# Optimization experiments

Measured on AMD Instinct MI355X. Metric: run time of the kernel, lower is better.

The kernel has to match this reference:

```python
import jax, jax.numpy as jnp
import numpy as np

B, IN_DIM, H, OUT_DIM = 2048, 1024, 256, 512   # batch, input_dim, hidden_dim, output_dim
T, K, HOPS = 12, 3, 4                            # num_tempers, ops per temper, max_path_hops


def setup_inputs() -> dict:
    key = jax.random.key(0)
    ks = jax.random.split(key, 10)
    s = 0.02
    return dict(
        x=jax.random.normal(ks[0], (B, IN_DIM), jnp.float32),
        init_tempers=jax.random.randint(ks[1], (B,), 0, T),
        op_noise=jax.random.normal(ks[2], (HOPS, T, K), jnp.float32),
        route_u=jax.random.uniform(ks[3], (HOPS, B, T + 1), jnp.float32),
        W_in=jax.random.normal(ks[4], (IN_DIM, H), jnp.float32) * s,
        b_in=jnp.zeros((H,), jnp.float32),
        W1=jax.random.normal(ks[5], (T, K, H, H), jnp.float32) * s,
        b1=jnp.zeros((T, K, H), jnp.float32),
        W2=jax.random.normal(ks[6], (T, K, H, H), jnp.float32) * s,
        b2=jnp.zeros((T, K, H), jnp.float32),
        Wr=jax.random.normal(ks[7], (T, H, T + 1), jnp.float32) * s,
        br=jnp.zeros((T, T + 1), jnp.float32),
        W_out=jax.random.normal(ks[8], (H, OUT_DIM), jnp.float32) * s,
        b_out=jnp.zeros((OUT_DIM,), jnp.float32),
    )


def reference(x, init_tempers, op_noise, route_u, W_in, b_in, W1, b1, W2, b2, Wr, br, W_out, b_out):
    # input projection; num_patches = hidden//hidden = 1, so patches == x_proj [N, H]
    states = x @ W_in + b_in                      # [N, H]
    N = states.shape[0]
    tempers = init_tempers                        # [N] in [0, T)
    done = jnp.zeros((N,), dtype=bool)

    for hop in range(HOPS):
        # per-temper operator mixing weights: softmax over randn(3) per Temper call
        w = jax.nn.softmax(op_noise[hop], axis=-1)                      # [T, K]
        # run all T expert MLPs densely (static-shape MoE dispatch), combine via one-hot
        h1 = jax.nn.relu(jnp.einsum('nh,tkhd->tnkd', states, W1) + b1[:, None])   # [T, N, K, H]
        h2 = jax.nn.relu(jnp.einsum('tnkd,tkdf->tnkf', h1, W2) + b2[:, None])     # [T, N, K, H]
        out_t = jnp.einsum('tnkf,tk->tnf', h2, w)                                  # [T, N, H]
        logits_t = jnp.einsum('tnf,tfg->tng', out_t, Wr) + br[:, None]             # [T, N, T+1]
        sel = jax.nn.one_hot(tempers, T, dtype=states.dtype)                       # [N, T]
        out = jnp.einsum('tnf,nt->nf', out_t, sel)                                 # [N, H]
        logits = jnp.einsum('tng,nt->ng', logits_t, sel)                           # [N, T+1]
        # multinomial(softmax(logits)) == argmax(logits + Gumbel)
        g = -jnp.log(-jnp.log(route_u[hop] + 1e-9) + 1e-9)
        sampled = jnp.argmax(logits + g, axis=-1)                                  # [N]
        active = ~done
        states = jnp.where(active[:, None], out, states)
        tempers = jnp.where(active, jnp.minimum(sampled, T - 1), tempers)
        done = done | (active & (sampled == T))

    # view(B, 1, H).mean(dim=1) is identity since num_patches == 1
    return states @ W_out + b_out
```

## Files before the change

kernel.cpp:

```cpp
#include <hip/hip_runtime.h>
#include <math.h>

#define BN_   2048
#define INDIM 1024
#define HD    256
#define OD    512
#define TN    12
#define KN    3
#define NHOPS 4
#define TP1   13

#define ER    8
#define CR    16

__device__ __forceinline__ void gll16(const float* g, float* l) {
  __builtin_amdgcn_global_load_lds(
      (const __attribute__((address_space(1))) void*)g,
      (__attribute__((address_space(3))) void*)l, 16, 0, 0);
}

__device__ __forceinline__ float4 ld4(const float* p) { return *(const float4*)p; }

__device__ __forceinline__ void fma4(float4& c, float a, const float4 b) {
  c.x = fmaf(a, b.x, c.x); c.y = fmaf(a, b.y, c.y);
  c.z = fmaf(a, b.z, c.z); c.w = fmaf(a, b.w, c.w);
}
__device__ __forceinline__ void add4(float4& c, const float4 b) {
  c.x += b.x; c.y += b.y; c.z += b.z; c.w += b.w;
}

template<int NR>
__device__ __forceinline__ void kloop(float4* acc, const float* SA, int astr,
                                      const float* w0, int ws, int nk4, int ks0) {
  const float* wp = w0;
  float4 wA0 = ld4(wp), wA1 = ld4(wp + ws), wA2 = ld4(wp + 2 * ws),
         wA3 = ld4(wp + 3 * ws);
#pragma unroll 1
  for (int k4 = 0; k4 < nk4 - 1; ++k4) {
    const float* wn = wp + 4 * ws;
    float4 wB0 = ld4(wn), wB1 = ld4(wn + ws), wB2 = ld4(wn + 2 * ws),
           wB3 = ld4(wn + 3 * ws);
    const int kk = ks0 + k4 * 4;
#pragma unroll
    for (int r = 0; r < NR; ++r) {
      float4 av = *(const float4*)(SA + r * astr + kk);
      fma4(acc[r], av.x, wA0); fma4(acc[r], av.y, wA1);
      fma4(acc[r], av.z, wA2); fma4(acc[r], av.w, wA3);
    }
    wA0 = wB0; wA1 = wB1; wA2 = wB2; wA3 = wB3; wp = wn;
  }
  const int kk = ks0 + (nk4 - 1) * 4;
#pragma unroll
  for (int r = 0; r < NR; ++r) {
    float4 av = *(const float4*)(SA + r * astr + kk);
    fma4(acc[r], av.x, wA0); fma4(acc[r], av.y, wA1);
    fma4(acc[r], av.z, wA2); fma4(acc[r], av.w, wA3);
  }
}

template<int NR>
__device__ __forceinline__ void reduce4(float4* acc, float4 (*pbA)[64],
                                        float4 (*pbB)[64], int w, int tx) {
  __syncthreads();
  if (w == 1) {
#pragma unroll
    for (int r = 0; r < NR; ++r) pbA[r][tx] = acc[r];
  } else if (w == 3) {
#pragma unroll
    for (int r = 0; r < NR; ++r) pbB[r][tx] = acc[r];
  }
  __syncthreads();
  if (w == 0) {
#pragma unroll
    for (int r = 0; r < NR; ++r) add4(acc[r], pbA[r][tx]);
  } else if (w == 2) {
#pragma unroll
    for (int r = 0; r < NR; ++r) add4(acc[r], pbB[r][tx]);
  }
  __syncthreads();
  if (w == 2) {
#pragma unroll
    for (int r = 0; r < NR; ++r) pbA[r][tx] = acc[r];
  }
  __syncthreads();
  if (w == 0) {
#pragma unroll
    for (int r = 0; r < NR; ++r) add4(acc[r], pbA[r][tx]);
  }
}

__global__ __launch_bounds__(256) void k_init(const int* __restrict__ init_t,
                                              int* __restrict__ cnt,
                                              int* __restrict__ gidx) {
  int n = blockIdx.x * 256 + threadIdx.x;
  if (n < BN_) {
    int t = init_t[n];
    int slot = atomicAdd(&cnt[t], 1);
    gidx[t * BN_ + slot] = n;
  }
}

__global__ __launch_bounds__(256) void k_gemm_in(const float* __restrict__ A,
                                                 const float* __restrict__ W,
                                                 float* __restrict__ pp) {
  const int bm = blockIdx.x * ER;
  const int kh = blockIdx.y;
  __shared__ float  sA[ER][512];
  __shared__ float4 pbA[ER][64];
  __shared__ float4 pbB[ER][64];
  const int tid = threadIdx.x;
  const int tx = tid & 63;
  const int w = tid >> 6;

#pragma unroll
  for (int l = 0; l < 4; ++l) {
    int idx = tid + l * 256;
    int r = idx >> 7;
    int c = (idx & 127) << 2;
    gll16(&A[(size_t)(bm + r) * INDIM + kh * 512 + c], &sA[r][c]);
  }
  __syncthreads();

  float4 acc[ER];
#pragma unroll
  for (int r = 0; r < ER; ++r) acc[r] = make_float4(0.f, 0.f, 0.f, 0.f);

  const int ks = w * 128;
  kloop<ER>(acc, &sA[0][0], 512, W + (size_t)(kh * 512 + ks) * HD + tx * 4, HD, 32, ks);
  reduce4<ER>(acc, pbA, pbB, w, tx);

  if (w == 0) {
#pragma unroll
    for (int r = 0; r < ER; ++r)
      *(float4*)&pp[((size_t)kh * BN_ + bm + r) * HD + tx * 4] = acc[r];
  }
}

__global__ __launch_bounds__(256) void k_cin(const float* __restrict__ pp,
                                             const float* __restrict__ bias,
                                             float* __restrict__ states) {
  int idx = blockIdx.x * 256 + threadIdx.x;
  int c = (idx & 63) << 2;
  float4 a = ld4(&pp[(size_t)idx * 4]);
  float4 b = ld4(&pp[(size_t)BN_ * HD + (size_t)idx * 4]);
  float4 bv = ld4(&bias[c]);
  float4 o = make_float4(a.x + b.x + bv.x, a.y + b.y + bv.y,
                         a.z + b.z + bv.z, a.w + b.w + bv.w);
  *(float4*)&states[(size_t)idx * 4] = o;
}

__global__ __launch_bounds__(256) void k_gemm_out(const float* __restrict__ A,
                                                  const float* __restrict__ W,
                                                  const float* __restrict__ bias,
                                                  float* __restrict__ C) {
  const int bm = blockIdx.x * ER;
  const int cb = blockIdx.y * 256;
  __shared__ float  sA[ER][HD];
  __shared__ float4 pbA[ER][64];
  __shared__ float4 pbB[ER][64];
  const int tid = threadIdx.x;
  const int tx = tid & 63;
  const int w = tid >> 6;

#pragma unroll
  for (int l = 0; l < 2; ++l) {
    int idx = tid + l * 256;
    int r = idx >> 6;
    int c = (idx & 63) << 2;
    gll16(&A[(size_t)(bm + r) * HD + c], &sA[r][c]);
  }
  __syncthreads();

  float4 acc[ER];
#pragma unroll
  for (int r = 0; r < ER; ++r) acc[r] = make_float4(0.f, 0.f, 0.f, 0.f);

  const int ks = w * 64;
  kloop<ER>(acc, &sA[0][0], HD, W + (size_t)ks * OD + cb + tx * 4, OD, 16, ks);
  reduce4<ER>(acc, pbA, pbB, w, tx);

  if (w == 0) {
    float4 bv = ld4(&bias[cb + tx * 4]);
#pragma unroll
    for (int r = 0; r < ER; ++r) {
      float4 o = make_float4(acc[r].x + bv.x, acc[r].y + bv.y,
                             acc[r].z + bv.z, acc[r].w + bv.w);
      *(float4*)&C[(size_t)(bm + r) * OD + cb + tx * 4] = o;
    }
  }
}

__global__ __launch_bounds__(256) void k_h1h2(
    int hop,
    const float* __restrict__ W1, const float* __restrict__ b1,
    const float* __restrict__ W2, const float* __restrict__ b2,
    const float* __restrict__ op_noise,
    const int* __restrict__ cnt, const int* __restrict__ gidx,
    const float* __restrict__ states, float* __restrict__ part) {
  const int t  = blockIdx.x % TN;
  const int rb = blockIdx.x / TN;
  const int k  = blockIdx.y;

  const int cntv = cnt[hop * 16 + t];
  const int r0 = rb * ER;
  if (r0 >= cntv) return;
  const int gb = (hop * TN + t) * BN_ + r0;
  const int rows = min(ER, cntv - r0);

  __shared__ float  sA[ER][HD];
  __shared__ float  sH[ER][HD];
  __shared__ float4 pbA[ER][64];
  __shared__ float4 pbB[ER][64];
  const int tid = threadIdx.x;
  const int tx = tid & 63;
  const int w = tid >> 6;

#pragma unroll
  for (int l = 0; l < 2; ++l) {
    int r = w + 4 * l;
    int c = tx << 2;
    if (r < rows)
      gll16(&states[(size_t)gidx[gb + r] * HD + c], &sA[r][c]);
  }
  __syncthreads();

  const float* Wa = W1 + (size_t)(t * KN + k) * HD * HD;
  const float* Wb = W2 + (size_t)(t * KN + k) * HD * HD;
  const int ks = w * 64;

  float4 acc[ER];
#pragma unroll
  for (int r = 0; r < ER; ++r) acc[r] = make_float4(0.f, 0.f, 0.f, 0.f);

  kloop<ER>(acc, &sA[0][0], HD, Wa + (size_t)ks * HD + tx * 4, HD, 16, ks);
  reduce4<ER>(acc, pbA, pbB, w, tx);

  if (w == 0) {
    float4 bv = ld4(&b1[(t * KN + k) * HD + tx * 4]);
#pragma unroll
    for (int r = 0; r < ER; ++r) {
      float4 h;
      h.x = fmaxf(acc[r].x + bv.x, 0.f);
      h.y = fmaxf(acc[r].y + bv.y, 0.f);
      h.z = fmaxf(acc[r].z + bv.z, 0.f);
      h.w = fmaxf(acc[r].w + bv.w, 0.f);
      *(float4*)&sH[r][tx * 4] = h;
    }
  }
  __syncthreads();

#pragma unroll
  for (int r = 0; r < ER; ++r) acc[r] = make_float4(0.f, 0.f, 0.f, 0.f);
  kloop<ER>(acc, &sH[0][0], HD, Wb + (size_t)ks * HD + tx * 4, HD, 16, ks);
  reduce4<ER>(acc, pbA, pbB, w, tx);

  if (w == 0) {
    float wkk;
    {
      const float* on = op_noise + (hop * TN + t) * KN;
      float x0 = on[0], x1 = on[1], x2 = on[2];
      float m = fmaxf(fmaxf(x0, x1), x2);
      float e0 = expf(x0 - m), e1 = expf(x1 - m), e2 = expf(x2 - m);
      float ek = (k == 0) ? e0 : (k == 1) ? e1 : e2;
      wkk = ek / (e0 + e1 + e2);
    }
    float4 bv = ld4(&b2[(t * KN + k) * HD + tx * 4]);
#pragma unroll
    for (int r = 0; r < ER; ++r) {
      if (r < rows) {
        int n = gidx[gb + r];
        float4 o;
        o.x = wkk * fmaxf(acc[r].x + bv.x, 0.f);
        o.y = wkk * fmaxf(acc[r].y + bv.y, 0.f);
        o.z = wkk * fmaxf(acc[r].z + bv.z, 0.f);
        o.w = wkk * fmaxf(acc[r].w + bv.w, 0.f);
        *(float4*)&part[((size_t)k * BN_ + n) * HD + tx * 4] = o;
      }
    }
  }
}

__global__ __launch_bounds__(256) void k_comb(
    int hop,
    const float* __restrict__ Wr, const float* __restrict__ br,
    const float* __restrict__ route_u,
    int* __restrict__ cnt, int* __restrict__ gidx,
    const float* __restrict__ part,
    float* __restrict__ states) {
  const int t  = blockIdx.x % TN;
  const int rb = blockIdx.x / TN;
  const int cntv = cnt[hop * 16 + t];
  const int r0 = rb * CR;
  if (r0 >= cntv) return;
  const int gb = (hop * TN + t) * BN_ + r0;
  const int rows = min(CR, cntv - r0);

  __shared__ float sO[CR][HD + 4];
  __shared__ float sWr[HD * TP1];
  __shared__ float sL[CR][16];
  __shared__ int   sN[CR];

  const int tid = threadIdx.x;
  if (tid < CR && tid < rows) sN[tid] = gidx[gb + tid];

#pragma unroll
  for (int l = 0; l < 4; ++l) {
    int idx = tid + l * 256;
    int r = idx >> 6;
    int c = (idx & 63) << 2;
    if (r < rows) {
      int n = gidx[gb + r];
      size_t p = (size_t)n * HD + c;
      float4 a = ld4(&part[p]);
      float4 b = ld4(&part[(size_t)BN_ * HD + p]);
      float4 cc = ld4(&part[(size_t)2 * BN_ * HD + p]);
      float4 v = make_float4(a.x + b.x + cc.x, a.y + b.y + cc.y,
                             a.z + b.z + cc.z, a.w + b.w + cc.w);
      *(float4*)&sO[r][c] = v;
      *(float4*)&states[(size_t)n * HD + c] = v;
    }
  }
  for (int i = tid; i < HD * TP1; i += 256)
    sWr[i] = Wr[(size_t)t * HD * TP1 + i];
  __syncthreads();

  int r = tid >> 4, g = tid & 15;
  if (r < rows && g < TP1) {
    float a = br[t * TP1 + g];
#pragma unroll 8
    for (int f = 0; f < HD; ++f) a = fmaf(sO[r][f], sWr[f * TP1 + g], a);
    float u = route_u[((size_t)hop * BN_ + sN[r]) * TP1 + g];
    float gb_ = -logf(-logf(u + 1e-9f) + 1e-9f);
    sL[r][g] = a + gb_;
  }
  __syncthreads();

  if (tid < rows) {
    float best = sL[tid][0];
    int bj = 0;
#pragma unroll
    for (int gg = 1; gg < TP1; ++gg) {
      float v = sL[tid][gg];
      if (v > best) { best = v; bj = gg; }
    }
    if (hop + 1 < NHOPS && bj != TN) {
      int n = sN[tid];
      int slot = atomicAdd(&cnt[(hop + 1) * 16 + bj], 1);
      gidx[((hop + 1) * TN + bj) * BN_ + slot] = n;
    }
  }
}

extern "C" void kernel_launch(void* const* d_in, const int* in_sizes, int n_in,
                              void* d_out, int out_size, void* d_ws, size_t ws_size,
                              hipStream_t stream) {
  const float* x        = (const float*)d_in[0];
  const int*   init_t   = (const int*)d_in[1];
  const float* op_noise = (const float*)d_in[2];
  const float* route_u  = (const float*)d_in[3];
  const float* W_in     = (const float*)d_in[4];
  const float* b_in     = (const float*)d_in[5];
  const float* W1       = (const float*)d_in[6];
  const float* b1       = (const float*)d_in[7];
  const float* W2       = (const float*)d_in[8];
  const float* b2       = (const float*)d_in[9];
  const float* Wr       = (const float*)d_in[10];
  const float* br       = (const float*)d_in[11];
  const float* W_out    = (const float*)d_in[12];
  const float* b_out    = (const float*)d_in[13];
  float* out = (float*)d_out;

  float* states = (float*)d_ws;
  float* part   = states + (size_t)BN_ * HD;
  float* pp     = part;
  int* cnt  = (int*)(part + (size_t)KN * BN_ * HD);
  int* gidx = cnt + NHOPS * 16;

  hipMemsetAsync(cnt, 0, NHOPS * 16 * sizeof(int), stream);
  k_init<<<(BN_ + 255) / 256, 256, 0, stream>>>(init_t, cnt, gidx);

  k_gemm_in<<<dim3(BN_ / ER, 2), 256, 0, stream>>>(x, W_in, pp);
  k_cin<<<(BN_ * HD / 4) / 256, 256, 0, stream>>>(pp, b_in, states);

  for (int hop = 0; hop < NHOPS; ++hop) {
    k_h1h2<<<dim3(TN * (BN_ / ER), KN), 256, 0, stream>>>(
        hop, W1, b1, W2, b2, op_noise, cnt, gidx, states, part);
    k_comb<<<TN * (BN_ / CR), 256, 0, stream>>>(
        hop, Wr, br, route_u, cnt, gidx, part, states);
  }

  k_gemm_out<<<dim3(BN_ / ER, OD / 256), 256, 0, stream>>>(states, W_out, b_out, out);
}
```

Before: 228.1 us.

## Double row tile, remap expert blocks across XCDs, fold count reset into init kernel

The rows per block go from 8 to 16 in all GEMM kernels, so each streamed weight tile is reused across twice as many rows. The expert MLP kernel moves to a 1D grid with an XCD-aware decode, so blocks of the same temper land on the same XCD and share L2 for its weights. The hidden activation buffer now aliases the reduction scratch to keep LDS usage down at the larger tile. The separate memset is folded into a single-block init kernel. The costs are more register pressure per thread, fewer blocks when some tempers have few rows, and reliance on the reduce barriers to keep the aliased buffer safe.

```diff
diff --git a/kernel.cpp b/kernel.cpp
--- a/kernel.cpp
+++ b/kernel.cpp
@@ -10,7 +10,7 @@
 #define NHOPS 4
 #define TP1   13
 
-#define ER    8
+#define ER    16
 #define CR    16
 
 __device__ __forceinline__ void gll16(const float* g, float* l) {
@@ -89,11 +89,13 @@
   }
 }
 
-__global__ __launch_bounds__(256) void k_init(const int* __restrict__ init_t,
-                                              int* __restrict__ cnt,
-                                              int* __restrict__ gidx) {
-  int n = blockIdx.x * 256 + threadIdx.x;
-  if (n < BN_) {
+__global__ __launch_bounds__(1024) void k_init(const int* __restrict__ init_t,
+                                               int* __restrict__ cnt,
+                                               int* __restrict__ gidx) {
+  const int tid = threadIdx.x;
+  if (tid < NHOPS * 16) cnt[tid] = 0;
+  __syncthreads();
+  for (int n = tid; n < BN_; n += 1024) {
     int t = init_t[n];
     int slot = atomicAdd(&cnt[t], 1);
     gidx[t * BN_ + slot] = n;
@@ -113,7 +115,7 @@
   const int w = tid >> 6;
 
 #pragma unroll
-  for (int l = 0; l < 4; ++l) {
+  for (int l = 0; l < 8; ++l) {
     int idx = tid + l * 256;
     int r = idx >> 7;
     int c = (idx & 127) << 2;
@@ -163,7 +165,7 @@
   const int w = tid >> 6;
 
 #pragma unroll
-  for (int l = 0; l < 2; ++l) {
+  for (int l = 0; l < 4; ++l) {
     int idx = tid + l * 256;
     int r = idx >> 6;
     int c = (idx & 63) << 2;
@@ -197,9 +199,16 @@
     const float* __restrict__ op_noise,
     const int* __restrict__ cnt, const int* __restrict__ gidx,
     const float* __restrict__ states, float* __restrict__ part) {
-  const int t  = blockIdx.x % TN;
-  const int rb = blockIdx.x / TN;
-  const int k  = blockIdx.y;
+  const int bid = blockIdx.x;
+  const int xcd = bid & 7;
+  const int s   = bid >> 3;
+  const int u   = xcd * 3 + (s % 3);
+  const int inner = s / 3;
+  const int k   = inner % 3;
+  const int j   = inner / 3;
+  const int t   = u >> 1;
+  const int h   = u & 1;
+  const int rb  = j * 2 + h;
 
   const int cntv = cnt[hop * 16 + t];
   const int r0 = rb * ER;
@@ -208,16 +217,16 @@
   const int rows = min(ER, cntv - r0);
 
   __shared__ float  sA[ER][HD];
-  __shared__ float  sH[ER][HD];
   __shared__ float4 pbA[ER][64];
   __shared__ float4 pbB[ER][64];
   const int tid = threadIdx.x;
   const int tx = tid & 63;
   const int w = tid >> 6;
-
-#pragma unroll
-  for (int l = 0; l < 2; ++l) {
-    int r = w + 4 * l;
+  float* sH = (float*)pbB;
+
+#pragma unroll
+  for (int l = 0; l < 4; ++l) {
+    int r = (tid >> 6) + 4 * l;
     int c = tx << 2;
     if (r < rows)
       gll16(&states[(size_t)gidx[gb + r] * HD + c], &sA[r][c]);
@@ -239,19 +248,19 @@
     float4 bv = ld4(&b1[(t * KN + k) * HD + tx * 4]);
 #pragma unroll
     for (int r = 0; r < ER; ++r) {
-      float4 h;
-      h.x = fmaxf(acc[r].x + bv.x, 0.f);
-      h.y = fmaxf(acc[r].y + bv.y, 0.f);
-      h.z = fmaxf(acc[r].z + bv.z, 0.f);
-      h.w = fmaxf(acc[r].w + bv.w, 0.f);
-      *(float4*)&sH[r][tx * 4] = h;
+      float4 hh;
+      hh.x = fmaxf(acc[r].x + bv.x, 0.f);
+      hh.y = fmaxf(acc[r].y + bv.y, 0.f);
+      hh.z = fmaxf(acc[r].z + bv.z, 0.f);
+      hh.w = fmaxf(acc[r].w + bv.w, 0.f);
+      *(float4*)&sH[r * HD + tx * 4] = hh;
     }
   }
   __syncthreads();
 
 #pragma unroll
   for (int r = 0; r < ER; ++r) acc[r] = make_float4(0.f, 0.f, 0.f, 0.f);
-  kloop<ER>(acc, &sH[0][0], HD, Wb + (size_t)ks * HD + tx * 4, HD, 16, ks);
+  kloop<ER>(acc, sH, HD, Wb + (size_t)ks * HD + tx * 4, HD, 16, ks);
   reduce4<ER>(acc, pbA, pbB, w, tx);
 
   if (w == 0) {
@@ -376,14 +385,13 @@
   int* cnt  = (int*)(part + (size_t)KN * BN_ * HD);
   int* gidx = cnt + NHOPS * 16;
 
-  hipMemsetAsync(cnt, 0, NHOPS * 16 * sizeof(int), stream);
-  k_init<<<(BN_ + 255) / 256, 256, 0, stream>>>(init_t, cnt, gidx);
+  k_init<<<1, 1024, 0, stream>>>(init_t, cnt, gidx);
 
   k_gemm_in<<<dim3(BN_ / ER, 2), 256, 0, stream>>>(x, W_in, pp);
   k_cin<<<(BN_ * HD / 4) / 256, 256, 0, stream>>>(pp, b_in, states);
 
   for (int hop = 0; hop < NHOPS; ++hop) {
-    k_h1h2<<<dim3(TN * (BN_ / ER), KN), 256, 0, stream>>>(
+    k_h1h2<<<8 * 3 * 3 * 64, 256, 0, stream>>>(
         hop, W1, b1, W2, b2, op_noise, cnt, gidx, states, part);
     k_comb<<<TN * (BN_ / CR), 256, 0, stream>>>(
         hop, Wr, br, route_u, cnt, gidx, part, states);
```

Measured after the change: 258.1 us. +13.2%, slower.
